# Optimization experiments

Hardware: AMD Instinct MI355X
Metric: run time of the kernel (lower is better)

Reference implementation:

```python
import jax, jax.numpy as jnp
import numpy as np

EMBED_DIM = 1024
NUM_HEADS = 16
HEAD_DIM = EMBED_DIM // NUM_HEADS


def setup_inputs() -> dict:
    key = jax.random.key(0)
    ks = jax.random.split(key, 9)
    B, N, D = 2, 2048, EMBED_DIM
    s = 1.0 / np.sqrt(D)
    return {
        "x": jax.random.normal(ks[0], (B, N, D), jnp.float32),
        "Wq": jax.random.normal(ks[1], (D, D), jnp.float32) * s,
        "bq": jax.random.normal(ks[2], (D,), jnp.float32) * 0.01,
        "Wk": jax.random.normal(ks[3], (D, D), jnp.float32) * s,
        "bk": jax.random.normal(ks[4], (D,), jnp.float32) * 0.01,
        "Wv": jax.random.normal(ks[5], (D, D), jnp.float32) * s,
        "bv": jax.random.normal(ks[6], (D,), jnp.float32) * 0.01,
        "Wo": jax.random.normal(ks[7], (D, D), jnp.float32) * s,
        "bo": jax.random.normal(ks[8], (D,), jnp.float32) * 0.01,
    }


def reference(x, Wq, bq, Wk, bk, Wv, bv, Wo, bo):
    B, N, D = x.shape
    H, Hd = NUM_HEADS, HEAD_DIM
    # QKV projections (Linear: x @ W^T + b), split heads -> [B, H, N, Hd]
    q = (x @ Wq.T + bq).reshape(B, N, H, Hd).transpose(0, 2, 1, 3)
    k = (x @ Wk.T + bk).reshape(B, N, H, Hd).transpose(0, 2, 1, 3)
    v = (x @ Wv.T + bv).reshape(B, N, H, Hd).transpose(0, 2, 1, 3)
    scale = 1.0 / np.sqrt(Hd)
    scores = jnp.einsum("bhqd,bhkd->bhqk", q, k) * scale  # [B,H,N,N]
    attn = jax.nn.softmax(scores.astype(jnp.float32), axis=-1).astype(scores.dtype)
    out = jnp.einsum("bhqk,bhkd->bhqd", attn, v)  # [B,H,N,Hd]
    out = out.transpose(0, 2, 1, 3).reshape(B, N, D)
    return out @ Wo.T + bo
```

## Files before the change

### kernel.cpp

```cpp
#include <hip/hip_runtime.h>
#include <hip/hip_bf16.h>

typedef __attribute__((ext_vector_type(8))) short short8;
typedef __attribute__((ext_vector_type(4))) float f32x4;
typedef __attribute__((ext_vector_type(4))) unsigned short us4;

static __device__ __forceinline__ unsigned short f2bf(float f) {
    union { float f; unsigned u; } v; v.f = f;
    unsigned r = (v.u + 0x7FFFu + ((v.u >> 16) & 1u)) >> 16;
    return (unsigned short)r;
}
static __device__ __forceinline__ unsigned pk2(float a, float b) {
    union { float f; unsigned u; } x, y; x.f = a; y.f = b;
    unsigned lo = (x.u + 0x7FFFu + ((x.u >> 16) & 1u)) >> 16;
    unsigned hi = (y.u + 0x7FFFu + ((y.u >> 16) & 1u)) >> 16;
    return lo | (hi << 16);
}
static __device__ __forceinline__ unsigned pk2f(float a, float b) {
    union { float f; unsigned u; } x, y; x.f = a; y.f = b;
    return ((x.u + 0x8000u) >> 16) | ((y.u + 0x8000u) & 0xFFFF0000u);
}

#if __has_builtin(__builtin_amdgcn_exp2f)
#define EXP2(x) __builtin_amdgcn_exp2f(x)
#else
#define EXP2(x) exp2f(x)
#endif

static __device__ __forceinline__ void gld16(const unsigned short* g, unsigned short* l) {
    __builtin_amdgcn_global_load_lds(
        (const __attribute__((address_space(1))) void*)g,
        (__attribute__((address_space(3))) void*)l, 16, 0, 0);
}

#define QSCALE (0.125f * 1.44269504f)

__global__ __launch_bounds__(256) void convert_all(
    const float* __restrict__ x,  const float* __restrict__ wq,
    const float* __restrict__ wk, const float* __restrict__ wv,
    const float* __restrict__ wo, const float* __restrict__ bq,
    const float* __restrict__ bk, const float* __restrict__ bv,
    unsigned short* __restrict__ xbf, unsigned short* __restrict__ wqkv,
    unsigned short* __restrict__ wobf, float* __restrict__ bqkv)
{
    const int NX4 = (4096 * 1024) / 4;
    const int NW4 = (1024 * 1024) / 4;
    int i = blockIdx.x * 256 + threadIdx.x;
    if (i < NX4) {
        float4 v = ((const float4*)x)[i];
        us4 o = { f2bf(v.x), f2bf(v.y), f2bf(v.z), f2bf(v.w) };
        ((us4*)xbf)[i] = o;
    } else if (i < NX4 + 3 * NW4) {
        int j = i - NX4;
        const float* src = (j < NW4) ? wq + 4 * j
                         : (j < 2 * NW4) ? wk + 4 * (j - NW4)
                         : wv + 4 * (j - 2 * NW4);
        float4 v = *(const float4*)src;
        us4 o = { f2bf(v.x), f2bf(v.y), f2bf(v.z), f2bf(v.w) };
        ((us4*)wqkv)[j] = o;
    } else if (i < NX4 + 4 * NW4) {
        int j = i - NX4 - 3 * NW4;
        float4 v = ((const float4*)wo)[j];
        us4 o = { f2bf(v.x), f2bf(v.y), f2bf(v.z), f2bf(v.w) };
        ((us4*)wobf)[j] = o;
    } else if (i < NX4 + 4 * NW4 + 768) {
        int j = i - NX4 - 4 * NW4;
        const float* src = (j < 256) ? bq + 4 * j
                         : (j < 512) ? bk + 4 * (j - 256)
                         : bv + 4 * (j - 512);
        ((float4*)bqkv)[j] = *(const float4*)src;
    }
}

template <int MODE, int BM, int BN, int WR, int WC>
__global__ __launch_bounds__(256) void gemm_bt(
    const unsigned short* __restrict__ A, const unsigned short* __restrict__ B,
    const float* __restrict__ bias,
    unsigned short* __restrict__ Qb, unsigned short* __restrict__ Kb,
    unsigned short* __restrict__ Vtb, float* __restrict__ Cout, int Mtiles)
{
    constexpr int WM = BM / WR, WN = BN / WC;
    constexpr int IT = WM / 16, JT = WN / 16;
    __shared__ __attribute__((aligned(16))) unsigned short As[BM * 64];
    __shared__ __attribute__((aligned(16))) unsigned short Bs[BN * 64];
    const int tid = threadIdx.x, lane = tid & 63;
    const int wave = tid >> 6;
    const int bm = blockIdx.x % Mtiles, bn = blockIdx.x / Mtiles;
    const int m0 = bm * BM, n0 = bn * BN;
    const int wr = wave / WC, wc = wave % WC;
    const int lo = lane & 15, g = lane >> 4;

    f32x4 acc[IT][JT];
#pragma unroll
    for (int i = 0; i < IT; ++i)
#pragma unroll
        for (int j = 0; j < JT; ++j) acc[i][j] = (f32x4){0.f, 0.f, 0.f, 0.f};

    for (int kt = 0; kt < 16; ++kt) {
        const int k0 = kt * 64;
#pragma unroll
        for (int p = 0; p < BM / 32; ++p) {
            int off = p * 2048 + tid * 8;
            int k8l = off / (BM * 8), m = (off >> 3) & (BM - 1);
            const unsigned short* srcA;
            if (MODE == 0) {
                srcA = A + (size_t)(m0 + m) * 1024 + k0 + k8l * 8;
            } else {
                int gr = m0 + m, b = gr >> 11, n = gr & 2047;
                srcA = A + ((size_t)((b << 4) + kt) * 2048 + n) * 64 + k8l * 8;
            }
            gld16(srcA, &As[off]);
        }
#pragma unroll
        for (int p = 0; p < BN / 32; ++p) {
            int off = p * 2048 + tid * 8;
            int k8l = off / (BN * 8), m = (off >> 3) & (BN - 1);
            gld16(B + (size_t)(n0 + m) * 1024 + k0 + k8l * 8, &Bs[off]);
        }
        __syncthreads();
        short8 af[IT][2], bf[JT][2];
#pragma unroll
        for (int kc = 0; kc < 2; ++kc) {
#pragma unroll
            for (int i = 0; i < IT; ++i)
                af[i][kc] = *(const short8*)&As[((kc * 4 + g) * BM + wr * WM + i * 16 + lo) * 8];
#pragma unroll
            for (int j = 0; j < JT; ++j)
                bf[j][kc] = *(const short8*)&Bs[((kc * 4 + g) * BN + wc * WN + j * 16 + lo) * 8];
        }
#pragma unroll
        for (int kc = 0; kc < 2; ++kc)
#pragma unroll
            for (int i = 0; i < IT; ++i)
#pragma unroll
                for (int j = 0; j < JT; ++j)
                    acc[i][j] = __builtin_amdgcn_mfma_f32_16x16x32_bf16(
                        af[i][kc], bf[j][kc], acc[i][j], 0, 0, 0);
        __syncthreads();
    }

    if (MODE == 0) {
        const int sect = n0 >> 10;
#pragma unroll
        for (int i = 0; i < IT; ++i)
#pragma unroll
            for (int j = 0; j < JT; ++j) {
                int gc = n0 + wc * WN + j * 16 + lo;
                int d = gc & 1023, h = d >> 6, hd = d & 63;
                float bv = bias[gc];
                int nb = m0 + wr * WM + i * 16 + g * 4;
                int b = nb >> 11, n = nb & 2047;
                size_t hb = (size_t)((b << 4) + h) * 131072;
                if (sect == 0) {
#pragma unroll
                    for (int r = 0; r < 4; ++r)
                        Qb[hb + (size_t)(n + r) * 64 + hd] =
                            f2bf((acc[i][j][r] + bv) * QSCALE);
                } else if (sect == 1) {
#pragma unroll
                    for (int r = 0; r < 4; ++r)
                        Kb[hb + (size_t)(hd >> 3) * 16384 + (size_t)(n + r) * 8 + (hd & 7)] =
                            f2bf(acc[i][j][r] + bv);
                } else {
                    uint2 w;
                    w.x = pk2(acc[i][j][0] + bv, acc[i][j][1] + bv);
                    w.y = pk2(acc[i][j][2] + bv, acc[i][j][3] + bv);
                    *(uint2*)&Vtb[hb + (size_t)(n >> 3) * 512 + (size_t)hd * 8 + (n & 7)] = w;
                }
            }
    } else {
#pragma unroll
        for (int i = 0; i < IT; ++i)
#pragma unroll
            for (int j = 0; j < JT; ++j)
#pragma unroll
                for (int r = 0; r < 4; ++r) {
                    int gr = m0 + wr * WM + i * 16 + g * 4 + r;
                    int gc = n0 + wc * WN + j * 16 + lo;
                    Cout[(size_t)gr * 1024 + gc] = acc[i][j][r] + bias[gc];
                }
    }
}

__global__ __launch_bounds__(256, 2) void attn_kernel(
    const unsigned short* __restrict__ Qb, const unsigned short* __restrict__ Kb,
    const unsigned short* __restrict__ Vtb, unsigned short* __restrict__ Ob)
{
    __shared__ __attribute__((aligned(16))) unsigned short PT[4 * 32 * 72];
    const int tid = threadIdx.x, lane = tid & 63, wave = tid >> 6;
    const int lo = lane & 15, g = lane >> 4;
    const int bh = blockIdx.x & 31, qt = blockIdx.x >> 5;
    const size_t base = (size_t)bh * 131072;
    const int q0w = qt * 128 + wave * 32;

    short8 aq[2][2];
#pragma unroll
    for (int rb = 0; rb < 2; ++rb) {
        const unsigned short* qp = Qb + base + (size_t)(q0w + rb * 16 + lo) * 64 + g * 8;
        aq[rb][0] = *(const short8*)qp;
        aq[rb][1] = *(const short8*)(qp + 32);
    }
    f32x4 o[2][4];
    float l[2] = {0.f, 0.f};
#pragma unroll
    for (int rb = 0; rb < 2; ++rb)
#pragma unroll
        for (int c = 0; c < 4; ++c) o[rb][c] = (f32x4){0.f, 0.f, 0.f, 0.f};
    unsigned short* myP = PT + wave * (32 * 72);

    const unsigned short* kb0 = Kb + base + (size_t)g * 16384 + (size_t)lo * 8;
    const unsigned short* kb1 = kb0 + 4 * 16384;
    const unsigned short* vb  = Vtb + base + (size_t)g * 512 + (size_t)lo * 8;

    short8 kf[2][8], vf[2][8];
    auto loadK = [&](int kt, short8* f) {
        const unsigned short* p0 = kb0 + kt * 512;
        const unsigned short* p1 = kb1 + kt * 512;
#pragma unroll
        for (int ct = 0; ct < 4; ++ct) {
            f[2 * ct]     = *(const short8*)(p0 + ct * 128);
            f[2 * ct + 1] = *(const short8*)(p1 + ct * 128);
        }
    };
    auto loadV = [&](int kt, short8* f) {
        const unsigned short* p = vb + (size_t)kt * 4096;
#pragma unroll
        for (int kc2 = 0; kc2 < 2; ++kc2)
#pragma unroll
            for (int c = 0; c < 4; ++c)
                f[kc2 * 4 + c] = *(const short8*)(p + kc2 * 2048 + c * 128);
    };

    loadK(0, kf[0]);
    loadV(0, vf[0]);

#pragma unroll 2
    for (int kt = 0; kt < 32; ++kt) {
        const int cur = kt & 1, nxt = cur ^ 1;
        const int ktn = (kt < 31) ? kt + 1 : 31;
        loadK(ktn, kf[nxt]);
#pragma unroll
        for (int ct = 0; ct < 4; ++ct) {
#pragma unroll
            for (int rb = 0; rb < 2; ++rb) {
                f32x4 z = (f32x4){0.f, 0.f, 0.f, 0.f};
                f32x4 s = __builtin_amdgcn_mfma_f32_16x16x32_bf16(kf[cur][2 * ct], aq[rb][0], z, 0, 0, 0);
                s = __builtin_amdgcn_mfma_f32_16x16x32_bf16(kf[cur][2 * ct + 1], aq[rb][1], s, 0, 0, 0);
                float p0 = EXP2(s[0]), p1 = EXP2(s[1]);
                float p2 = EXP2(s[2]), p3 = EXP2(s[3]);
                l[rb] += (p0 + p1) + (p2 + p3);
                uint2 w; w.x = pk2f(p0, p1); w.y = pk2f(p2, p3);
                *(uint2*)&myP[(rb * 16 + lo) * 72 + ct * 16 + g * 4] = w;
            }
        }
        loadV(ktn, vf[nxt]);
#pragma unroll
        for (int kc2 = 0; kc2 < 2; ++kc2) {
            short8 bp0 = *(const short8*)&myP[lo * 72 + kc2 * 32 + g * 8];
            short8 bp1 = *(const short8*)&myP[(16 + lo) * 72 + kc2 * 32 + g * 8];
#pragma unroll
            for (int c = 0; c < 4; ++c) {
                short8 v8 = vf[cur][kc2 * 4 + c];
                o[0][c] = __builtin_amdgcn_mfma_f32_16x16x32_bf16(v8, bp0, o[0][c], 0, 0, 0);
                o[1][c] = __builtin_amdgcn_mfma_f32_16x16x32_bf16(v8, bp1, o[1][c], 0, 0, 0);
            }
        }
    }

    float inv[2];
#pragma unroll
    for (int rb = 0; rb < 2; ++rb) {
        float v = l[rb];
        v += __shfl_xor(v, 16);
        v += __shfl_xor(v, 32);
        inv[rb] = 1.f / v;
    }
#pragma unroll
    for (int rb = 0; rb < 2; ++rb)
#pragma unroll
        for (int c = 0; c < 4; ++c) {
            uint2 w;
            w.x = pk2(o[rb][c][0] * inv[rb], o[rb][c][1] * inv[rb]);
            w.y = pk2(o[rb][c][2] * inv[rb], o[rb][c][3] * inv[rb]);
            *(uint2*)&Ob[base + (size_t)(q0w + rb * 16 + lo) * 64 + c * 16 + g * 4] = w;
        }
}

extern "C" void kernel_launch(void* const* d_in, const int* in_sizes, int n_in,
                              void* d_out, int out_size, void* d_ws, size_t ws_size,
                              hipStream_t stream) {
    const float* x  = (const float*)d_in[0];
    const float* Wq = (const float*)d_in[1];
    const float* bq = (const float*)d_in[2];
    const float* Wk = (const float*)d_in[3];
    const float* bk = (const float*)d_in[4];
    const float* Wv = (const float*)d_in[5];
    const float* bv = (const float*)d_in[6];
    const float* Wo = (const float*)d_in[7];
    const float* bo = (const float*)d_in[8];
    float* out = (float*)d_out;

    char* ws = (char*)d_ws;
    unsigned short* xbf  = (unsigned short*)ws;
    unsigned short* wqkv = (unsigned short*)(ws + 8388608);
    unsigned short* wobf = (unsigned short*)(ws + 14680064);
    float*          bqkv = (float*)(ws + 16777216);
    unsigned short* Qb   = (unsigned short*)(ws + 16789504);
    unsigned short* Kb   = (unsigned short*)(ws + 16789504 + 8388608);
    unsigned short* Vtb  = (unsigned short*)(ws + 16789504 + 2 * 8388608);
    unsigned short* Ob   = (unsigned short*)(ws + 16789504 + 3 * 8388608);

    convert_all<<<8195, 256, 0, stream>>>(x, Wq, Wk, Wv, Wo, bq, bk, bv,
                                          xbf, wqkv, wobf, bqkv);
    gemm_bt<0, 128, 128, 2, 2><<<32 * 24, 256, 0, stream>>>(
        xbf, wqkv, bqkv, Qb, Kb, Vtb, nullptr, 32);
    attn_kernel<<<512, 256, 0, stream>>>(Qb, Kb, Vtb, Ob);
    gemm_bt<1, 64, 64, 2, 2><<<64 * 16, 256, 0, stream>>>(
        Ob, wobf, bo, nullptr, nullptr, nullptr, out, 64);
}
```

Before: 232.3 us.

## Replace LDS-staged GEMM with direct global-to-register double-buffered loads

The projection GEMMs no longer stage tiles through shared memory with global_load_lds and barriers. Each wave now loads its MFMA fragments straight from global memory into registers and double-buffers them across k-steps. The QKV GEMM tile also shrinks to 128x64 with twice as many blocks, and launch bounds ask for 2 blocks per CU. This removes the LDS round trip and syncthreads, but each wave loses cross-wave data reuse, so global and L2 traffic grows and the 16-byte per-lane loads are less coalesced.

```diff
diff --git a/kernel.cpp b/kernel.cpp
--- a/kernel.cpp
+++ b/kernel.cpp
@@ -26,12 +26,6 @@
 #else
 #define EXP2(x) exp2f(x)
 #endif
-
-static __device__ __forceinline__ void gld16(const unsigned short* g, unsigned short* l) {
-    __builtin_amdgcn_global_load_lds(
-        (const __attribute__((address_space(1))) void*)g,
-        (__attribute__((address_space(3))) void*)l, 16, 0, 0);
-}
 
 #define QSCALE (0.125f * 1.44269504f)
 
@@ -73,7 +67,7 @@
 }
 
 template <int MODE, int BM, int BN, int WR, int WC>
-__global__ __launch_bounds__(256) void gemm_bt(
+__global__ __launch_bounds__(256, 2) void gemm_direct(
     const unsigned short* __restrict__ A, const unsigned short* __restrict__ B,
     const float* __restrict__ bias,
     unsigned short* __restrict__ Qb, unsigned short* __restrict__ Kb,
@@ -81,53 +75,55 @@
 {
     constexpr int WM = BM / WR, WN = BN / WC;
     constexpr int IT = WM / 16, JT = WN / 16;
-    __shared__ __attribute__((aligned(16))) unsigned short As[BM * 64];
-    __shared__ __attribute__((aligned(16))) unsigned short Bs[BN * 64];
-    const int tid = threadIdx.x, lane = tid & 63;
-    const int wave = tid >> 6;
+    const int tid = threadIdx.x, lane = tid & 63, wave = tid >> 6;
     const int bm = blockIdx.x % Mtiles, bn = blockIdx.x / Mtiles;
     const int m0 = bm * BM, n0 = bn * BN;
     const int wr = wave / WC, wc = wave % WC;
     const int lo = lane & 15, g = lane >> 4;
 
+    unsigned offA[IT], offB[JT];
+#pragma unroll
+    for (int i = 0; i < IT; ++i) {
+        int row = m0 + wr * WM + i * 16 + lo;
+        if (MODE == 0) {
+            offA[i] = (unsigned)row * 1024 + g * 8;
+        } else {
+            int b = row >> 11, n = row & 2047;
+            offA[i] = (unsigned)b * 2097152 + (unsigned)n * 64 + g * 8;
+        }
+    }
+#pragma unroll
+    for (int j = 0; j < JT; ++j)
+        offB[j] = (unsigned)(n0 + wc * WN + j * 16 + lo) * 1024 + g * 8;
+
     f32x4 acc[IT][JT];
 #pragma unroll
     for (int i = 0; i < IT; ++i)
 #pragma unroll
         for (int j = 0; j < JT; ++j) acc[i][j] = (f32x4){0.f, 0.f, 0.f, 0.f};
 
+    short8 af[2][IT][2], bf[2][JT][2];
+    auto load = [&](int kt, int buf) {
+#pragma unroll
+        for (int i = 0; i < IT; ++i) {
+            unsigned o = (MODE == 0) ? offA[i] + kt * 64 : offA[i] + kt * 131072;
+            af[buf][i][0] = *(const short8*)(A + o);
+            af[buf][i][1] = *(const short8*)(A + o + 32);
+        }
+#pragma unroll
+        for (int j = 0; j < JT; ++j) {
+            unsigned o = offB[j] + kt * 64;
+            bf[buf][j][0] = *(const short8*)(B + o);
+            bf[buf][j][1] = *(const short8*)(B + o + 32);
+        }
+    };
+
+    load(0, 0);
+#pragma unroll 2
     for (int kt = 0; kt < 16; ++kt) {
-        const int k0 = kt * 64;
-#pragma unroll
-        for (int p = 0; p < BM / 32; ++p) {
-            int off = p * 2048 + tid * 8;
-            int k8l = off / (BM * 8), m = (off >> 3) & (BM - 1);
-            const unsigned short* srcA;
-            if (MODE == 0) {
-                srcA = A + (size_t)(m0 + m) * 1024 + k0 + k8l * 8;
-            } else {
-                int gr = m0 + m, b = gr >> 11, n = gr & 2047;
-                srcA = A + ((size_t)((b << 4) + kt) * 2048 + n) * 64 + k8l * 8;
-            }
-            gld16(srcA, &As[off]);
-        }
-#pragma unroll
-        for (int p = 0; p < BN / 32; ++p) {
-            int off = p * 2048 + tid * 8;
-            int k8l = off / (BN * 8), m = (off >> 3) & (BN - 1);
-            gld16(B + (size_t)(n0 + m) * 1024 + k0 + k8l * 8, &Bs[off]);
-        }
-        __syncthreads();
-        short8 af[IT][2], bf[JT][2];
-#pragma unroll
-        for (int kc = 0; kc < 2; ++kc) {
-#pragma unroll
-            for (int i = 0; i < IT; ++i)
-                af[i][kc] = *(const short8*)&As[((kc * 4 + g) * BM + wr * WM + i * 16 + lo) * 8];
-#pragma unroll
-            for (int j = 0; j < JT; ++j)
-                bf[j][kc] = *(const short8*)&Bs[((kc * 4 + g) * BN + wc * WN + j * 16 + lo) * 8];
-        }
+        const int cur = kt & 1, nxt = cur ^ 1;
+        const int ktn = (kt < 15) ? kt + 1 : 15;
+        load(ktn, nxt);
 #pragma unroll
         for (int kc = 0; kc < 2; ++kc)
 #pragma unroll
@@ -135,8 +131,7 @@
 #pragma unroll
                 for (int j = 0; j < JT; ++j)
                     acc[i][j] = __builtin_amdgcn_mfma_f32_16x16x32_bf16(
-                        af[i][kc], bf[j][kc], acc[i][j], 0, 0, 0);
-        __syncthreads();
+                        af[cur][i][kc], bf[cur][j][kc], acc[i][j], 0, 0, 0);
     }
 
     if (MODE == 0) {
@@ -312,9 +307,9 @@
 
     convert_all<<<8195, 256, 0, stream>>>(x, Wq, Wk, Wv, Wo, bq, bk, bv,
                                           xbf, wqkv, wobf, bqkv);
-    gemm_bt<0, 128, 128, 2, 2><<<32 * 24, 256, 0, stream>>>(
+    gemm_direct<0, 128, 64, 2, 2><<<32 * 48, 256, 0, stream>>>(
         xbf, wqkv, bqkv, Qb, Kb, Vtb, nullptr, 32);
     attn_kernel<<<512, 256, 0, stream>>>(Qb, Kb, Vtb, Ob);
-    gemm_bt<1, 64, 64, 2, 2><<<64 * 16, 256, 0, stream>>>(
+    gemm_direct<1, 64, 64, 2, 2><<<64 * 16, 256, 0, stream>>>(
         Ob, wobf, bo, nullptr, nullptr, nullptr, out, 64);
 }
```

Result: slower. 342.9 us (+47.6%).
